# Optimization experiments

Hardware: AMD Instinct MI355X
Metric: run time of the kernel (lower is better)

## Reference

```python
import jax, jax.numpy as jnp
import numpy as np

S, N, F, H, O = 64, 4096, 32, 64, 2  # seq_len, n_nodes, nfeat, nhid, nout


def setup_inputs() -> dict:
    key = jax.random.key(0)
    ks = jax.random.split(key, 8)
    sc = 0.02
    return {
        "x": jax.random.normal(ks[0], (S, N, F), jnp.float32),
        "adj": jax.random.uniform(ks[1], (N, N), jnp.float32) / N,  # dense normalized-ish adjacency
        "W1": jax.random.normal(ks[2], (F, H), jnp.float32) * sc,
        "b1": jnp.zeros((H,), jnp.float32),
        "W2": jax.random.normal(ks[3], (H, O), jnp.float32) * sc,
        "b2": jnp.zeros((O,), jnp.float32),
        "Wih0": jax.random.normal(ks[4], (3 * H, O * N), jnp.float32) * sc,
        "Whh0": jax.random.normal(ks[5], (3 * H, H), jnp.float32) * sc,
        "bih0": jnp.zeros((3 * H,), jnp.float32),
        "bhh0": jnp.zeros((3 * H,), jnp.float32),
        "Wih1": jax.random.normal(ks[6], (3 * H, H), jnp.float32) * sc,
        "Whh1": jax.random.normal(ks[7], (3 * H, H), jnp.float32) * sc,
        "bih1": jnp.zeros((3 * H,), jnp.float32),
        "bhh1": jnp.zeros((3 * H,), jnp.float32),
    }


def _gru_layer(xs, Wih, Whh, bih, bhh):
    # xs: (S, B, in); PyTorch GRU cell semantics, h0 = 0
    B = xs.shape[1]
    h0 = jnp.zeros((B, Whh.shape[1]), xs.dtype)

    def step(h, x_t):
        gi = x_t @ Wih.T + bih            # (B, 3H)
        gh = h @ Whh.T + bhh              # (B, 3H)
        ir, iz, inn = jnp.split(gi, 3, axis=-1)
        hr, hz, hn = jnp.split(gh, 3, axis=-1)
        r = jax.nn.sigmoid(ir + hr)
        z = jax.nn.sigmoid(iz + hz)
        n = jnp.tanh(inn + r * hn)
        h_new = (1.0 - z) * n + z * h
        return h_new, h_new

    hT, ys = jax.lax.scan(step, h0, xs)
    return ys, hT


def reference(x, adj, W1, b1, W2, b2, Wih0, Whh0, bih0, bhh0, Wih1, Whh1, bih1, bhh1):
    # GCN per timestep (vectorized over time): adj @ (x @ W) + b, relu, adj @ (. @ W2) + b2, log_softmax
    # dropout inactive (eval mode)
    support = jnp.einsum('snf,fh->snh', x, W1) + b1          # (S, N, H)
    h = jnp.einsum('ij,sjh->sih', adj, support)              # (S, N, H)
    h = jax.nn.relu(h)
    support2 = jnp.einsum('snh,ho->sno', h, W2) + b2         # (S, N, O)
    g = jnp.einsum('ij,sjo->sio', adj, support2)             # (S, N, O)
    logp = jax.nn.log_softmax(g, axis=-1)                    # dim=1 of (N, O) per node
    rnn_in = logp.reshape(S, 1, N * O)                       # batch = 1 (torch.stack construction)
    ys0, h0T = _gru_layer(rnn_in, Wih0, Whh0, bih0, bhh0)
    ys1, h1T = _gru_layer(ys0, Wih1, Whh1, bih1, bhh1)
    hn = jnp.stack([h0T, h1T])                               # (n_layers, 1, H)
    return ys1, hn
```

## Files before the change

kernel.cpp:

```cpp
#include <hip/hip_runtime.h>
#include <stdint.h>

#define SS 64
#define NN 4096
#define FF 32
#define HH 64
#define OO 2
#define G3 192

typedef float f32x4 __attribute__((ext_vector_type(4)));
typedef short bf16x8 __attribute__((ext_vector_type(8)));
typedef unsigned short u16x8 __attribute__((ext_vector_type(8)));
typedef long longx2 __attribute__((ext_vector_type(2)));

#define AS1 __attribute__((address_space(1)))
#define AS3 __attribute__((address_space(3)))

__device__ __forceinline__ unsigned short f2bf(float f) {
  union { float f; uint32_t u; } v; v.f = f;
  uint32_t u = v.u;
  uint32_t r = (u + 0x7FFFu + ((u >> 16) & 1u)) >> 16;
  return (unsigned short)r;
}
__device__ __forceinline__ float bf2f(unsigned short s) {
  union { uint32_t u; float f; } v; v.u = ((uint32_t)s) << 16;
  return v.f;
}
__device__ __forceinline__ unsigned char f2e4m3(float x) {
  float a = fabsf(x);
  unsigned s = (x < 0.f) ? 0x80u : 0u;
  if (a >= 448.f) return (unsigned char)(s | 0x7E);
  if (a < 0.015625f) {
    int q = (int)rintf(a * 512.f);
    return (unsigned char)(s | (unsigned)q);
  }
  union { float f; uint32_t u; } v; v.f = a;
  uint32_t b = v.u + 0x7FFFFu + ((v.u >> 20) & 1u);
  int e = (int)(b >> 23) - 127;
  if (e > 8) return (unsigned char)(s | 0x7E);
  return (unsigned char)(s | (unsigned)(((e + 7) << 3) | ((b >> 20) & 7u)));
}

__global__ __launch_bounds__(256) void k_prep(const float* __restrict__ adj,
                                              unsigned short* __restrict__ adjb,
                                              unsigned char* __restrict__ adj8,
                                              float* __restrict__ rowsum,
                                              const float* __restrict__ x,
                                              unsigned char* __restrict__ Xt8) {
  __shared__ float xl[64][33];
  __shared__ float ps[4];
  int tid = threadIdx.x;
  if (blockIdx.x < 4096) {
    int row = blockIdx.x;
    const float4* src = (const float4*)(adj + (size_t)row * 4096);
    ushort4* dst = (ushort4*)(adjb + (size_t)row * 4096);
    uchar4* dst8 = (uchar4*)(adj8 + (size_t)row * 4096);
    float sum = 0.f;
    #pragma unroll
    for (int q = 0; q < 4; ++q) {
      int idx = q * 256 + tid;
      float4 v = src[idx];
      ushort4 r;
      r.x = f2bf(v.x); r.y = f2bf(v.y); r.z = f2bf(v.z); r.w = f2bf(v.w);
      dst[idx] = r;
      uchar4 r8;
      r8.x = f2e4m3(v.x * 4096.f); r8.y = f2e4m3(v.y * 4096.f);
      r8.z = f2e4m3(v.z * 4096.f); r8.w = f2e4m3(v.w * 4096.f);
      int o8 = (idx >> 1) & 7;
      int np = ((o8 & 3) << 1) | (o8 >> 2);
      int nidx = (idx & ~15) | (np << 1) | (idx & 1);
      dst8[nidx] = r8;
      sum += (v.x + v.y) + (v.z + v.w);
    }
    #pragma unroll
    for (int off = 1; off < 64; off <<= 1) sum += __shfl_xor(sum, off);
    if ((tid & 63) == 0) ps[tid >> 6] = sum;
    __syncthreads();
    if (tid == 0) rowsum[row] = (ps[0] + ps[1]) + (ps[2] + ps[3]);
    return;
  }
  int bs = blockIdx.x - 4096;
  int s = bs >> 6, jb = (bs & 63) << 6;
  const float4* xg = (const float4*)(x + ((size_t)s * NN + jb) * FF);
  #pragma unroll
  for (int ii = 0; ii < 2; ++ii) {
    int idx = tid + ii * 256;
    float4 v = xg[idx];
    int j = idx >> 3, f = (idx & 7) << 2;
    xl[j][f] = v.x; xl[j][f + 1] = v.y; xl[j][f + 2] = v.z; xl[j][f + 3] = v.w;
  }
  __syncthreads();
  int f = tid >> 3, jc = tid & 7;
  unsigned int lo = 0, hi = 0;
  #pragma unroll
  for (int jj = 0; jj < 4; ++jj) lo |= ((unsigned int)f2e4m3(xl[jc * 8 + jj][f])) << (jj * 8);
  #pragma unroll
  for (int jj = 0; jj < 4; ++jj) hi |= ((unsigned int)f2e4m3(xl[jc * 8 + 4 + jj][f])) << (jj * 8);
  uint2 ov; ov.x = lo; ov.y = hi;
  int np = ((jc & 3) << 1) | (jc >> 2);
  *(uint2*)(Xt8 + (size_t)(s * 32 + f) * 4096 + jb + np * 8) = ov;
}

#define SBAR()   asm volatile("s_barrier" ::: "memory")
#define VMC9()   asm volatile("s_waitcnt vmcnt(9)" ::: "memory")
#define VMC6()   asm volatile("s_waitcnt vmcnt(6)" ::: "memory")
#define VMC3()   asm volatile("s_waitcnt vmcnt(3)" ::: "memory")
#define VMC0()   asm volatile("s_waitcnt vmcnt(0)" ::: "memory")

__global__ __launch_bounds__(512, 2) void k_gemmAX(
    const unsigned char* __restrict__ A8,
    const unsigned char* __restrict__ B8,
    const float* __restrict__ rowsum,
    const float* __restrict__ W1f,
    const float* __restrict__ b1f,
    const float* __restrict__ W2f,
    const float* __restrict__ b2f,
    unsigned short* __restrict__ B2t) {
  __shared__ __align__(16) char lds[122880];
  __shared__ __align__(16) unsigned short w1t[64 * 40];
  __shared__ float w2l[128];
  __shared__ float b1l[64];
  __shared__ float b2l[2];
  const int tid = threadIdx.x;
  const int wid = tid >> 6, l = tid & 63;
  const int wr2 = wid >> 2, wc2 = wid & 3;
  const int lc = l & 15, lq = l >> 4;

  {
    float4 v = ((const float4*)W1f)[tid];
    int f = tid >> 4, h = (tid & 15) * 4;
    w1t[(h + 0) * 40 + f] = f2bf(v.x);
    w1t[(h + 1) * 40 + f] = f2bf(v.y);
    w1t[(h + 2) * 40 + f] = f2bf(v.z);
    w1t[(h + 3) * 40 + f] = f2bf(v.w);
  }
  if (tid < 32) *(float4*)&w2l[tid * 4] = ((const float4*)W2f)[tid];
  if (tid < 16) *(float4*)&b1l[tid * 4] = ((const float4*)b1f)[tid];
  if (tid < 2) b2l[tid] = b2f[tid];
  __syncthreads();

  int bid = blockIdx.x;
  int swz = (bid & 7) * 32 + (bid >> 3);
  const int i0 = (swz >> 3) * 128;
  const int c0 = (swz & 7) * 256;

  const int aBase = (wr2 * 64 + lc) * 64;
  const int bBase = 8192 + (wc2 * 64 + lc) * 64;
  const int aswz = (lc & 3) ^ ((lc >> 2) & 3);
  const int ckx = ((lq ^ aswz) << 4);

  const int srow = wid * 16 + (l >> 2);
  const int sswz = (srow & 3) ^ ((srow >> 2) & 3);
  const int scol = (((l & 3) ^ sswz) << 4);
  const char* gA = (const char*)A8 + (size_t)(i0 + srow) * 4096 + scol;
  const char* gB = (const char*)B8 + (size_t)(c0 + srow) * 4096 + scol;
  char* ldsW = (char*)lds + wid * 1024;
  const char* ldsR = (const char*)lds;

  f32x4 acc[4][4];
  #pragma unroll
  for (int m = 0; m < 4; ++m)
    #pragma unroll
    for (int n = 0; n < 4; ++n) acc[m][n] = {0.f, 0.f, 0.f, 0.f};

  longx2 afq[4], bfq[4];

#define STAGE3(KT, BOFS) do {                                                        \
    __builtin_amdgcn_global_load_lds((const AS1 void*)(gA + (KT) * 64),              \
        (AS3 void*)(ldsW + (BOFS)), 16, 0, 0);                                       \
    __builtin_amdgcn_global_load_lds((const AS1 void*)(gB + (KT) * 64),              \
        (AS3 void*)(ldsW + (BOFS) + 8192), 16, 0, 0);                                \
    __builtin_amdgcn_global_load_lds((const AS1 void*)(gB + 524288 + (KT) * 64),     \
        (AS3 void*)(ldsW + (BOFS) + 16384), 16, 0, 0);                               \
  } while (0)

#define READ_FR(BOFS) do {                                                           \
    _Pragma("unroll")                                                                \
    for (int _m = 0; _m < 4; ++_m)                                                   \
      afq[_m] = *(const longx2*)(ldsR + (BOFS) + aBase + _m * 1024 + ckx);           \
    _Pragma("unroll")                                                                \
    for (int _n = 0; _n < 4; ++_n)                                                   \
      bfq[_n] = *(const longx2*)(ldsR + (BOFS) + bBase + _n * 1024 + ckx);           \
  } while (0)

#define MFMA32() do {                                                                \
    __builtin_amdgcn_s_setprio(1);                                                   \
    _Pragma("unroll")                                                                \
    for (int _kk = 0; _kk < 2; ++_kk)                                                \
      _Pragma("unroll")                                                              \
      for (int _m = 0; _m < 4; ++_m)                                                 \
        _Pragma("unroll")                                                            \
        for (int _n = 0; _n < 4; ++_n)                                               \
          acc[_m][_n] = __builtin_amdgcn_mfma_f32_16x16x32_fp8_fp8(                  \
              afq[_m][_kk], bfq[_n][_kk], acc[_m][_n], 0, 0, 0);                     \
    __builtin_amdgcn_s_setprio(0);                                                   \
  } while (0)

  STAGE3(0, 0);
  STAGE3(1, 24576);
  STAGE3(2, 49152);
  STAGE3(3, 73728);
  VMC9();
  SBAR();

  int bR = 0, bS = 98304;
  for (int kt = 0; kt < 60; ++kt) {
    READ_FR(bR);
    STAGE3(kt + 4, bS);
    MFMA32();
    VMC9();
    SBAR();
    bR = (bR == 98304) ? 0 : bR + 24576;
    bS = (bS == 98304) ? 0 : bS + 24576;
  }
  READ_FR(bR); MFMA32(); VMC6(); SBAR(); bR = (bR == 98304) ? 0 : bR + 24576;
  READ_FR(bR); MFMA32(); VMC3(); SBAR(); bR = (bR == 98304) ? 0 : bR + 24576;
  READ_FR(bR); MFMA32(); VMC0(); SBAR(); bR = (bR == 98304) ? 0 : bR + 24576;
  READ_FR(bR); MFMA32();
  __syncthreads();

  unsigned short* C1L = (unsigned short*)lds;
  {
    const int rb = wr2 * 64 + lq * 4;
    const int cbL = wc2 * 64 + lc;
    #pragma unroll
    for (int m = 0; m < 4; ++m)
      #pragma unroll
      for (int r = 0; r < 4; ++r) {
        const int row = rb + m * 16 + r;
        #pragma unroll
        for (int n = 0; n < 4; ++n)
          C1L[row * 264 + cbL + n * 16] = f2bf(acc[m][n][r] * 0.000244140625f);
      }
  }
  __syncthreads();

  {
    const f32x4 zacc = {0.f, 0.f, 0.f, 0.f};
    bf16x8 bw[4];
    float b1v[4], w2a[4], w2b[4];
    #pragma unroll
    for (int n = 0; n < 4; ++n) {
      const int h = n * 16 + lc;
      bw[n] = *(const bf16x8*)((const char*)w1t + h * 80 + lq * 16);
      b1v[n] = b1l[h];
      w2a[n] = w2l[h * 2];
      w2b[n] = w2l[h * 2 + 1];
    }
    const int rbase = wid * 16 + lq * 4;
    const float4 rs4 = *(const float4*)&rowsum[i0 + rbase];
    const float bo0 = b2l[0], bo1 = b2l[1];
    #pragma unroll
    for (int s = 0; s < 8; ++s) {
      bf16x8 afe = *(const bf16x8*)((const char*)C1L +
                     (wid * 16 + lc) * 528 + s * 64 + lq * 16);
      float o0r[4] = {0.f, 0.f, 0.f, 0.f};
      float o1r[4] = {0.f, 0.f, 0.f, 0.f};
      #pragma unroll
      for (int n = 0; n < 4; ++n) {
        f32x4 hq = __builtin_amdgcn_mfma_f32_16x16x32_bf16(afe, bw[n], zacc, 0, 0, 0);
        #pragma unroll
        for (int r = 0; r < 4; ++r) {
          float hv = hq[r] + rs4[r] * b1v[n];
          hv = hv > 0.f ? hv : 0.f;
          o0r[r] += hv * w2a[n];
          o1r[r] += hv * w2b[n];
        }
      }
      #pragma unroll
      for (int off = 1; off < 16; off <<= 1)
        #pragma unroll
        for (int r = 0; r < 4; ++r) {
          o0r[r] += __shfl_xor(o0r[r], off);
          o1r[r] += __shfl_xor(o1r[r], off);
        }
      if (lc == 0) {
        const int sg = (c0 >> 5) + s;
        #pragma unroll
        for (int r = 0; r < 4; ++r) {
          B2t[(size_t)(sg * 2 + 0) * 4096 + i0 + rbase + r] = f2bf(o0r[r] + bo0);
          B2t[(size_t)(sg * 2 + 1) * 4096 + i0 + rbase + r] = f2bf(o1r[r] + bo1);
        }
      }
    }
  }
}

__device__ __forceinline__ void gemm_core(const unsigned short* __restrict__ A,
                                          const unsigned short* __restrict__ B,
                                          int i0, int c0, int k0base, int ksteps,
                                          f32x4 acc[4][4],
                                          unsigned short* Als, unsigned short* Bls) {
  const int tid = threadIdx.x;
  const int w = tid >> 6, l = tid & 63;
  const int srow = (l >> 2);
  const int scol = (l & 3) * 16;
  for (int kt = 0; kt < ksteps; ++kt) {
    int k0 = k0base + kt * 32;
    #pragma unroll
    for (int q = 0; q < 2; ++q) {
      int r = w * 32 + q * 16 + srow;
      const char* ga = (const char*)(A + (size_t)(i0 + r) * 4096 + k0) + scol;
      __builtin_amdgcn_global_load_lds(
          (const AS1 void*)ga,
          (AS3 void*)((char*)Als + w * 2048 + q * 1024), 16, 0, 0);
      const char* gb = (const char*)(B + (size_t)(c0 + r) * 4096 + k0) + scol;
      __builtin_amdgcn_global_load_lds(
          (const AS1 void*)gb,
          (AS3 void*)((char*)Bls + w * 2048 + q * 1024), 16, 0, 0);
    }
    __syncthreads();
    const int wr = w >> 1, wc = w & 1;
    bf16x8 af[4], bff[4];
    #pragma unroll
    for (int m = 0; m < 4; ++m)
      af[m] = *(const bf16x8*)(Als + (wr * 64 + m * 16 + (l & 15)) * 32 + (l >> 4) * 8);
    #pragma unroll
    for (int n = 0; n < 4; ++n)
      bff[n] = *(const bf16x8*)(Bls + (wc * 64 + n * 16 + (l & 15)) * 32 + (l >> 4) * 8);
    #pragma unroll
    for (int m = 0; m < 4; ++m)
      #pragma unroll
      for (int n = 0; n < 4; ++n)
        acc[m][n] = __builtin_amdgcn_mfma_f32_16x16x32_bf16(af[m], bff[n], acc[m][n], 0, 0, 0);
    __syncthreads();
  }
}

__global__ __launch_bounds__(256) void k_gemm2(const unsigned short* __restrict__ A,
                                               const unsigned short* __restrict__ B,
                                               float* __restrict__ Gp) {
  __shared__ unsigned short Als[128 * 32], Bls[128 * 32];
  int id = blockIdx.x;
  int bi = id & 31, ks = id >> 5;
  int i0 = bi * 128;
  f32x4 acc[4][4];
  #pragma unroll
  for (int m = 0; m < 4; ++m)
    #pragma unroll
    for (int n = 0; n < 4; ++n) acc[m][n] = {0.f, 0.f, 0.f, 0.f};
  gemm_core(A, B, i0, 0, ks * 512, 16, acc, Als, Bls);
  float* outp = Gp + (size_t)ks * 4096 * 128;
  int l = threadIdx.x & 63, w = threadIdx.x >> 6;
  int wr = w >> 1, wc = w & 1;
  int rbase = i0 + wr * 64 + (l >> 4) * 4;
  int cbase = wc * 64 + (l & 15);
  #pragma unroll
  for (int m = 0; m < 4; ++m)
    #pragma unroll
    for (int n = 0; n < 4; ++n)
      #pragma unroll
      for (int r = 0; r < 4; ++r)
        outp[(size_t)(rbase + m * 16 + r) * 128 + cbase + n * 16] = acc[m][n][r];
}

__global__ __launch_bounds__(256) void k_lsm(const float* __restrict__ Gp,
                                             float* __restrict__ Rm) {
  __shared__ float Gacc[32][130];
  int i0 = blockIdx.x * 32;
  int tid = threadIdx.x;
  float4 v[4];
  #pragma unroll
  for (int i = 0; i < 4; ++i) v[i] = {0.f, 0.f, 0.f, 0.f};
  for (int ks = 0; ks < 8; ++ks) {
    const float4* gp4 = ((const float4*)Gp) + (size_t)ks * 131072 + (size_t)i0 * 32;
    #pragma unroll
    for (int i = 0; i < 4; ++i) {
      float4 t = gp4[tid + i * 256];
      v[i].x += t.x; v[i].y += t.y; v[i].z += t.z; v[i].w += t.w;
    }
  }
  #pragma unroll
  for (int i = 0; i < 4; ++i) {
    int f4i = tid + i * 256, row = f4i >> 5, c = (f4i & 31) * 4;
    Gacc[row][c] = v[i].x; Gacc[row][c + 1] = v[i].y;
    Gacc[row][c + 2] = v[i].z; Gacc[row][c + 3] = v[i].w;
  }
  __syncthreads();
  #pragma unroll
  for (int j = 0; j < 8; ++j) {
    int p = j * 256 + tid;
    int ii = p & 31, s = p >> 5;
    float g0 = Gacc[ii][s * 2], g1 = Gacc[ii][s * 2 + 1];
    float m = fmaxf(g0, g1);
    float lse = m + logf(expf(g0 - m) + expf(g1 - m));
    float2 o_; o_.x = g0 - lse; o_.y = g1 - lse;
    *((float2*)(Rm + (size_t)s * 8192 + (size_t)(i0 + ii) * 2)) = o_;
  }
}

__global__ __launch_bounds__(256) void k_gi0(const float* __restrict__ Rm,
                                             const float* __restrict__ Wih0,
                                             float* __restrict__ part) {
  __shared__ float4 Wl[4 * 128];
  int gb = blockIdx.x % 48, ks = blockIdx.x / 48;
  int c0 = ks * 512;
  int tid = threadIdx.x;
  #pragma unroll
  for (int i = 0; i < 2; ++i) {
    int idx = tid + i * 256;
    int g = idx >> 7, c4 = idx & 127;
    Wl[g * 128 + c4] = ((const float4*)(Wih0 + (size_t)(gb * 4 + g) * 8192 + c0))[c4];
  }
  __syncthreads();
  int w = tid >> 6, lane = tid & 63;
  for (int pass = 0; pass < 16; ++pass) {
    int t = pass * 4 + w;
    float a0 = 0.f, a1 = 0.f, a2 = 0.f, a3 = 0.f;
    const float4* rg = (const float4*)(Rm + (size_t)t * 8192 + c0);
    #pragma unroll
    for (int i = 0; i < 2; ++i) {
      int c4 = i * 64 + lane;
      float4 r4 = rg[c4];
      float4 w0 = Wl[c4], w1 = Wl[128 + c4], w2 = Wl[256 + c4], w3 = Wl[384 + c4];
      a0 += r4.x * w0.x + r4.y * w0.y + r4.z * w0.z + r4.w * w0.w;
      a1 += r4.x * w1.x + r4.y * w1.y + r4.z * w1.z + r4.w * w1.w;
      a2 += r4.x * w2.x + r4.y * w2.y + r4.z * w2.z + r4.w * w2.w;
      a3 += r4.x * w3.x + r4.y * w3.y + r4.z * w3.z + r4.w * w3.w;
    }
    #pragma unroll
    for (int off = 1; off < 64; off <<= 1) {
      a0 += __shfl_xor(a0, off);
      a1 += __shfl_xor(a1, off);
      a2 += __shfl_xor(a2, off);
      a3 += __shfl_xor(a3, off);
    }
    if (lane == 0) {
      float4 o_; o_.x = a0; o_.y = a1; o_.z = a2; o_.w = a3;
      *((float4*)(part + ((size_t)ks * 64 + t) * 192 + gb * 4)) = o_;
    }
  }
}

__global__ __launch_bounds__(256) void k_gi0red(const float* __restrict__ part,
                                                const float* __restrict__ bih0,
                                                float* __restrict__ gi0) {
  int idx = blockIdx.x * 256 + threadIdx.x;
  if (idx < 12288) {
    float s_ = bih0[idx % 192];
    for (int ks = 0; ks < 16; ++ks) s_ += part[ks * 12288 + idx];
    gi0[idx] = s_;
  }
}

__device__ __forceinline__ float fsigm(float x) {
  return __builtin_amdgcn_rcpf(1.f + __expf(-x));
}
__device__ __forceinline__ float ftanh(float x) {
  return 1.f - 2.f * __builtin_amdgcn_rcpf(1.f + __expf(2.f * x));
}

__global__ __launch_bounds__(384) void k_gru(const float* __restrict__ gi0,
                                             const float* __restrict__ Whh0,
                                             const float* __restrict__ bhh0,
                                             const float* __restrict__ Wih1,
                                             const float* __restrict__ Whh1,
                                             const float* __restrict__ bih1,
                                             const float* __restrict__ bhh1,
                                             float* __restrict__ out) {
  __shared__ float gil[64][192];
  __shared__ float gout[576];
  __shared__ __align__(16) unsigned short hv[2][64];
  const int tid = threadIdx.x;
  const int w = tid >> 6, l = tid & 63;
  const int matw = w >> 1, half = w & 1;
  const float* Wm = (matw == 0) ? Whh0 : (matw == 1 ? Wih1 : Whh1);
  const int mi = (matw == 2) ? 1 : 0;

  bf16x8 afr[6][2];
  #pragma unroll
  for (int rbi = 0; rbi < 6; ++rbi) {
    int g = (half * 6 + rbi) * 16 + (l & 15);
    #pragma unroll
    for (int kh = 0; kh < 2; ++kh) {
      int k0 = kh * 32 + (l >> 4) * 8;
      const float4* src = (const float4*)(Wm + (size_t)g * 64 + k0);
      float4 v0 = src[0], v1 = src[1];
      bf16x8 a;
      a[0] = (short)f2bf(v0.x); a[1] = (short)f2bf(v0.y);
      a[2] = (short)f2bf(v0.z); a[3] = (short)f2bf(v0.w);
      a[4] = (short)f2bf(v1.x); a[5] = (short)f2bf(v1.y);
      a[6] = (short)f2bf(v1.z); a[7] = (short)f2bf(v1.w);
      afr[rbi][kh] = a;
    }
  }
  {
    float4* gf = (float4*)&gil[0][0];
    const float4* gs = (const float4*)gi0;
    #pragma unroll
    for (int i = 0; i < 8; ++i) gf[i * 384 + tid] = gs[i * 384 + tid];
  }
  if (tid < 128) hv[tid >> 6][tid & 63] = 0;

  float hreg = 0.f;
  float bR = 0.f, bZ = 0.f, bNa = 0.f, bNb = 0.f;
  if (tid < 64) {
    bR = bhh0[tid]; bZ = bhh0[64 + tid]; bNa = bhh0[128 + tid];
  } else if (tid < 128) {
    int g = tid - 64;
    bR = bih1[g] + bhh1[g];
    bZ = bih1[64 + g] + bhh1[64 + g];
    bNa = bih1[128 + g];
    bNb = bhh1[128 + g];
  }
  asm volatile("s_waitcnt lgkmcnt(0)\n\ts_barrier" ::: "memory");

  const int gwb = matw * 192 + half * 96 + (l >> 4) * 4;
  const f32x4 zacc = {0.f, 0.f, 0.f, 0.f};

  for (int i = 0; i <= 64; ++i) {
    bf16x8 b0 = *(const bf16x8*)&hv[mi][(l >> 4) * 8];
    bf16x8 b1 = *(const bf16x8*)&hv[mi][32 + (l >> 4) * 8];
    #pragma unroll
    for (int rbi = 0; rbi < 6; ++rbi) {
      f32x4 a_ = __builtin_amdgcn_mfma_f32_16x16x32_bf16(afr[rbi][0], b0, zacc, 0, 0, 0);
      a_ = __builtin_amdgcn_mfma_f32_16x16x32_bf16(afr[rbi][1], b1, a_, 0, 0, 0);
      if (!(l & 15)) *(f32x4*)&gout[gwb + rbi * 16] = a_;
    }
    asm volatile("s_waitcnt lgkmcnt(0)\n\ts_barrier" ::: "memory");
    if (tid < 64) {
      if (i < 64) {
        float r = fsigm(gil[i][tid] + gout[tid] + bR);
        float z = fsigm(gil[i][64 + tid] + gout[64 + tid] + bZ);
        float n = ftanh(gil[i][128 + tid] + r * (gout[128 + tid] + bNa));
        hreg = (1.f - z) * n + z * hreg;
        hv[0][tid] = f2bf(hreg);
      }
    } else if (tid < 128 && i > 0) {
      int g = tid - 64;
      float r = fsigm(gout[192 + g] + gout[384 + g] + bR);
      float z = fsigm(gout[256 + g] + gout[448 + g] + bZ);
      float n = ftanh((gout[320 + g] + bNa) + r * (gout[512 + g] + bNb));
      hreg = (1.f - z) * n + z * hreg;
      hv[1][g] = f2bf(hreg);
      out[(i - 1) * 64 + g] = hreg;
    }
    asm volatile("s_waitcnt lgkmcnt(0)\n\ts_barrier" ::: "memory");
  }
  if (tid < 64) out[4096 + tid] = hreg;
  else if (tid < 128) out[4096 + 64 + (tid - 64)] = hreg;
}

extern "C" void kernel_launch(void* const* d_in, const int* in_sizes, int n_in,
                              void* d_out, int out_size, void* d_ws, size_t ws_size,
                              hipStream_t stream) {
  const float* x    = (const float*)d_in[0];
  const float* adj  = (const float*)d_in[1];
  const float* W1   = (const float*)d_in[2];
  const float* b1   = (const float*)d_in[3];
  const float* W2   = (const float*)d_in[4];
  const float* b2   = (const float*)d_in[5];
  const float* Wih0 = (const float*)d_in[6];
  const float* Whh0 = (const float*)d_in[7];
  const float* bih0 = (const float*)d_in[8];
  const float* bhh0 = (const float*)d_in[9];
  const float* Wih1 = (const float*)d_in[10];
  const float* Whh1 = (const float*)d_in[11];
  const float* bih1 = (const float*)d_in[12];
  const float* bhh1 = (const float*)d_in[13];
  float* out = (float*)d_out;

  char* ws = (char*)d_ws;
  unsigned short* adjb = (unsigned short*)ws;
  unsigned char* adj8  = (unsigned char*)(ws + 33554432);
  unsigned char* Xt8   = (unsigned char*)(ws + 50331648);
  float* rowsum        = (float*)(ws + 58720256);
  float* Gp            = (float*)(ws + 58736640);
  float* Rm            = (float*)(ws + 75513856);
  float* part          = (float*)(ws + 77611008);
  float* gi0           = (float*)(ws + 78397440);
  unsigned short* B2t  = (unsigned short*)(ws + 78446592);

  k_prep<<<8192, 256, 0, stream>>>(adj, adjb, adj8, rowsum, x, Xt8);
  k_gemmAX<<<256, 512, 0, stream>>>(adj8, Xt8, rowsum, W1, b1, W2, b2, B2t);
  k_gemm2<<<256, 256, 0, stream>>>(adjb, B2t, Gp);
  k_lsm<<<128, 256, 0, stream>>>(Gp, Rm);
  k_gi0<<<768, 256, 0, stream>>>(Rm, Wih0, part);
  k_gi0red<<<48, 256, 0, stream>>>(part, bih0, gi0);
  k_gru<<<1, 384, 0, stream>>>(gi0, Whh0, bhh0, Wih1, Whh1, bih1, bhh1, out);
}
```

Measured before the change: 158.6 us.

## Run second adjacency GEMM in FP8 and drop bf16 adjacency copy

```diff
diff --git a/kernel.cpp b/kernel.cpp
--- a/kernel.cpp
+++ b/kernel.cpp
@@ -40,9 +40,13 @@
   if (e > 8) return (unsigned char)(s | 0x7E);
   return (unsigned char)(s | (unsigned)(((e + 7) << 3) | ((b >> 20) & 7u)));
 }
+__device__ __forceinline__ int kperm_idx(int i) {
+  int o8 = (i >> 3) & 7;
+  int np = ((o8 & 3) << 1) | (o8 >> 2);
+  return (i & ~63) | (np << 3) | (i & 7);
+}
 
 __global__ __launch_bounds__(256) void k_prep(const float* __restrict__ adj,
-                                              unsigned short* __restrict__ adjb,
                                               unsigned char* __restrict__ adj8,
                                               float* __restrict__ rowsum,
                                               const float* __restrict__ x,
@@ -53,16 +57,12 @@
   if (blockIdx.x < 4096) {
     int row = blockIdx.x;
     const float4* src = (const float4*)(adj + (size_t)row * 4096);
-    ushort4* dst = (ushort4*)(adjb + (size_t)row * 4096);
     uchar4* dst8 = (uchar4*)(adj8 + (size_t)row * 4096);
     float sum = 0.f;
     #pragma unroll
     for (int q = 0; q < 4; ++q) {
       int idx = q * 256 + tid;
       float4 v = src[idx];
-      ushort4 r;
-      r.x = f2bf(v.x); r.y = f2bf(v.y); r.z = f2bf(v.z); r.w = f2bf(v.w);
-      dst[idx] = r;
       uchar4 r8;
       r8.x = f2e4m3(v.x * 4096.f); r8.y = f2e4m3(v.y * 4096.f);
       r8.z = f2e4m3(v.z * 4096.f); r8.w = f2e4m3(v.w * 4096.f);
@@ -104,6 +104,7 @@
 #define SBAR()   asm volatile("s_barrier" ::: "memory")
 #define VMC9()   asm volatile("s_waitcnt vmcnt(9)" ::: "memory")
 #define VMC6()   asm volatile("s_waitcnt vmcnt(6)" ::: "memory")
+#define VMC4()   asm volatile("s_waitcnt vmcnt(4)" ::: "memory")
 #define VMC3()   asm volatile("s_waitcnt vmcnt(3)" ::: "memory")
 #define VMC0()   asm volatile("s_waitcnt vmcnt(0)" ::: "memory")
 
@@ -115,7 +116,7 @@
     const float* __restrict__ b1f,
     const float* __restrict__ W2f,
     const float* __restrict__ b2f,
-    unsigned short* __restrict__ B2t) {
+    unsigned char* __restrict__ B2t8) {
   __shared__ __align__(16) char lds[122880];
   __shared__ __align__(16) unsigned short w1t[64 * 40];
   __shared__ float w2l[128];
@@ -278,80 +279,111 @@
         const int sg = (c0 >> 5) + s;
         #pragma unroll
         for (int r = 0; r < 4; ++r) {
-          B2t[(size_t)(sg * 2 + 0) * 4096 + i0 + rbase + r] = f2bf(o0r[r] + bo0);
-          B2t[(size_t)(sg * 2 + 1) * 4096 + i0 + rbase + r] = f2bf(o1r[r] + bo1);
+          const int ip = kperm_idx(i0 + rbase + r);
+          B2t8[(size_t)(sg * 2 + 0) * 4096 + ip] = f2e4m3((o0r[r] + bo0) * 4096.f);
+          B2t8[(size_t)(sg * 2 + 1) * 4096 + ip] = f2e4m3((o1r[r] + bo1) * 4096.f);
         }
       }
     }
   }
 }
 
-__device__ __forceinline__ void gemm_core(const unsigned short* __restrict__ A,
-                                          const unsigned short* __restrict__ B,
-                                          int i0, int c0, int k0base, int ksteps,
-                                          f32x4 acc[4][4],
-                                          unsigned short* Als, unsigned short* Bls) {
+__global__ __launch_bounds__(256) void k_gemm2f8(
+    const unsigned char* __restrict__ A8,
+    const unsigned char* __restrict__ B8,
+    float* __restrict__ Gp) {
+  __shared__ __align__(16) char lds[49152];
   const int tid = threadIdx.x;
-  const int w = tid >> 6, l = tid & 63;
-  const int srow = (l >> 2);
-  const int scol = (l & 3) * 16;
-  for (int kt = 0; kt < ksteps; ++kt) {
-    int k0 = k0base + kt * 32;
-    #pragma unroll
-    for (int q = 0; q < 2; ++q) {
-      int r = w * 32 + q * 16 + srow;
-      const char* ga = (const char*)(A + (size_t)(i0 + r) * 4096 + k0) + scol;
-      __builtin_amdgcn_global_load_lds(
-          (const AS1 void*)ga,
-          (AS3 void*)((char*)Als + w * 2048 + q * 1024), 16, 0, 0);
-      const char* gb = (const char*)(B + (size_t)(c0 + r) * 4096 + k0) + scol;
-      __builtin_amdgcn_global_load_lds(
-          (const AS1 void*)gb,
-          (AS3 void*)((char*)Bls + w * 2048 + q * 1024), 16, 0, 0);
-    }
-    __syncthreads();
-    const int wr = w >> 1, wc = w & 1;
-    bf16x8 af[4], bff[4];
-    #pragma unroll
-    for (int m = 0; m < 4; ++m)
-      af[m] = *(const bf16x8*)(Als + (wr * 64 + m * 16 + (l & 15)) * 32 + (l >> 4) * 8);
-    #pragma unroll
-    for (int n = 0; n < 4; ++n)
-      bff[n] = *(const bf16x8*)(Bls + (wc * 64 + n * 16 + (l & 15)) * 32 + (l >> 4) * 8);
-    #pragma unroll
-    for (int m = 0; m < 4; ++m)
-      #pragma unroll
-      for (int n = 0; n < 4; ++n)
-        acc[m][n] = __builtin_amdgcn_mfma_f32_16x16x32_bf16(af[m], bff[n], acc[m][n], 0, 0, 0);
-    __syncthreads();
-  }
-}
-
-__global__ __launch_bounds__(256) void k_gemm2(const unsigned short* __restrict__ A,
-                                               const unsigned short* __restrict__ B,
-                                               float* __restrict__ Gp) {
-  __shared__ unsigned short Als[128 * 32], Bls[128 * 32];
-  int id = blockIdx.x;
-  int bi = id & 31, ks = id >> 5;
-  int i0 = bi * 128;
+  const int wid = tid >> 6, l = tid & 63;
+  const int wr = wid >> 1, wc = wid & 1;
+  const int lc = l & 15, lq = l >> 4;
+  const int bi = blockIdx.x & 31, ks = blockIdx.x >> 5;
+  const int i0 = bi * 128;
+  const size_t kbase = (size_t)ks * 512;
+
+  const int aBase = (wr * 64 + lc) * 64;
+  const int bBase = 8192 + (wc * 64 + lc) * 64;
+  const int aswz = (lc & 3) ^ ((lc >> 2) & 3);
+  const int ckx = ((lq ^ aswz) << 4);
+
+  const int srow = wid * 16 + (l >> 2);
+  const int sswz = (srow & 3) ^ ((srow >> 2) & 3);
+  const int scol = (((l & 3) ^ sswz) << 4);
+  const char* gA = (const char*)A8 + (size_t)(i0 + srow) * 4096 + kbase + scol;
+  const char* gB = (const char*)B8 + (size_t)srow * 4096 + kbase + scol;
+  char* ldsW = (char*)lds + wid * 1024;
+  const char* ldsR = (const char*)lds;
+
   f32x4 acc[4][4];
   #pragma unroll
   for (int m = 0; m < 4; ++m)
     #pragma unroll
     for (int n = 0; n < 4; ++n) acc[m][n] = {0.f, 0.f, 0.f, 0.f};
-  gemm_core(A, B, i0, 0, ks * 512, 16, acc, Als, Bls);
-  float* outp = Gp + (size_t)ks * 4096 * 128;
-  int l = threadIdx.x & 63, w = threadIdx.x >> 6;
-  int wr = w >> 1, wc = w & 1;
-  int rbase = i0 + wr * 64 + (l >> 4) * 4;
-  int cbase = wc * 64 + (l & 15);
+
+  longx2 afq[4], bfq[4];
+
+#define G2STAGE(KT, BOFS) do {                                                       \
+    __builtin_amdgcn_global_load_lds((const AS1 void*)(gA + (KT) * 64),              \
+        (AS3 void*)(ldsW + (BOFS)), 16, 0, 0);                                       \
+    __builtin_amdgcn_global_load_lds((const AS1 void*)(gA + 262144 + (KT) * 64),     \
+        (AS3 void*)(ldsW + (BOFS) + 4096), 16, 0, 0);                                \
+    __builtin_amdgcn_global_load_lds((const AS1 void*)(gB + (KT) * 64),              \
+        (AS3 void*)(ldsW + (BOFS) + 8192), 16, 0, 0);                                \
+    __builtin_amdgcn_global_load_lds((const AS1 void*)(gB + 262144 + (KT) * 64),     \
+        (AS3 void*)(ldsW + (BOFS) + 12288), 16, 0, 0);                               \
+  } while (0)
+
+#define G2READ(BOFS) do {                                                            \
+    _Pragma("unroll")                                                                \
+    for (int _m = 0; _m < 4; ++_m)                                                   \
+      afq[_m] = *(const longx2*)(ldsR + (BOFS) + aBase + _m * 1024 + ckx);           \
+    _Pragma("unroll")                                                                \
+    for (int _n = 0; _n < 4; ++_n)                                                   \
+      bfq[_n] = *(const longx2*)(ldsR + (BOFS) + bBase + _n * 1024 + ckx);           \
+  } while (0)
+
+#define G2MFMA() do {                                                                \
+    __builtin_amdgcn_s_setprio(1);                                                   \
+    _Pragma("unroll")                                                                \
+    for (int _kk = 0; _kk < 2; ++_kk)                                                \
+      _Pragma("unroll")                                                              \
+      for (int _m = 0; _m < 4; ++_m)                                                 \
+        _Pragma("unroll")                                                            \
+        for (int _n = 0; _n < 4; ++_n)                                               \
+          acc[_m][_n] = __builtin_amdgcn_mfma_f32_16x16x32_fp8_fp8(                  \
+              afq[_m][_kk], bfq[_n][_kk], acc[_m][_n], 0, 0, 0);                     \
+    __builtin_amdgcn_s_setprio(0);                                                   \
+  } while (0)
+
+  G2STAGE(0, 0);
+  G2STAGE(1, 16384);
+  VMC4();
+  SBAR();
+
+  int bR = 0, bS = 32768;
+  for (int kt = 0; kt < 6; ++kt) {
+    G2READ(bR);
+    G2STAGE(kt + 2, bS);
+    G2MFMA();
+    VMC4();
+    SBAR();
+    bR = (bR == 32768) ? 0 : bR + 16384;
+    bS = (bS == 32768) ? 0 : bS + 16384;
+  }
+  G2READ(bR); G2MFMA(); VMC0(); SBAR(); bR = (bR == 32768) ? 0 : bR + 16384;
+  G2READ(bR); G2MFMA();
+
+  float* outp = Gp + (size_t)ks * 524288;
+  const int rbase = i0 + wr * 64 + lq * 4;
+  const int cbase = wc * 64 + lc;
   #pragma unroll
   for (int m = 0; m < 4; ++m)
     #pragma unroll
     for (int n = 0; n < 4; ++n)
       #pragma unroll
       for (int r = 0; r < 4; ++r)
-        outp[(size_t)(rbase + m * 16 + r) * 128 + cbase + n * 16] = acc[m][n][r];
+        outp[(size_t)(rbase + m * 16 + r) * 128 + cbase + n * 16] =
+            acc[m][n][r] * 5.9604644775390625e-8f;
 }
 
 __global__ __launch_bounds__(256) void k_lsm(const float* __restrict__ Gp,
@@ -561,19 +593,18 @@
   float* out = (float*)d_out;
 
   char* ws = (char*)d_ws;
-  unsigned short* adjb = (unsigned short*)ws;
-  unsigned char* adj8  = (unsigned char*)(ws + 33554432);
-  unsigned char* Xt8   = (unsigned char*)(ws + 50331648);
-  float* rowsum        = (float*)(ws + 58720256);
-  float* Gp            = (float*)(ws + 58736640);
-  float* Rm            = (float*)(ws + 75513856);
-  float* part          = (float*)(ws + 77611008);
-  float* gi0           = (float*)(ws + 78397440);
-  unsigned short* B2t  = (unsigned short*)(ws + 78446592);
-
-  k_prep<<<8192, 256, 0, stream>>>(adj, adjb, adj8, rowsum, x, Xt8);
-  k_gemmAX<<<256, 512, 0, stream>>>(adj8, Xt8, rowsum, W1, b1, W2, b2, B2t);
-  k_gemm2<<<256, 256, 0, stream>>>(adjb, B2t, Gp);
+  unsigned char* adj8  = (unsigned char*)ws;
+  unsigned char* Xt8   = (unsigned char*)(ws + 16777216);
+  float* rowsum        = (float*)(ws + 25165824);
+  float* Gp            = (float*)(ws + 25182208);
+  float* Rm            = (float*)(ws + 41959424);
+  float* part          = (float*)(ws + 44056576);
+  float* gi0           = (float*)(ws + 44843008);
+  unsigned char* B2t8  = (unsigned char*)(ws + 44892160);
+
+  k_prep<<<8192, 256, 0, stream>>>(adj, adj8, rowsum, x, Xt8);
+  k_gemmAX<<<256, 512, 0, stream>>>(adj8, Xt8, rowsum, W1, b1, W2, b2, B2t8);
+  k_gemm2f8<<<256, 256, 0, stream>>>(adj8, B2t8, Gp);
   k_lsm<<<128, 256, 0, stream>>>(Gp, Rm);
   k_gi0<<<768, 256, 0, stream>>>(Rm, Wih0, part);
   k_gi0red<<<48, 256, 0, stream>>>(part, bih0, gi0);
```

Result: faster. 151.5 us (-4.5%).
